# Kernel optimization log

Measured on AMD Instinct MI355X. Metric: run time of the kernel, lower is better.

Reference implementation:

```python
import jax, jax.numpy as jnp
import numpy as np

N = 32768
E = 8           # num_submodules (4x2 grid)
HID = 256       # hidden_dim
POS_DIM = 63    # 3*(1+2*10)
DIR_DIM = 27    # 3*(1+2*4)
APP_DIM = 48
IN_DIM = POS_DIM + APP_DIM        # 111
SKIP_IN = HID + IN_DIM            # 367
COL_IN = HID + DIR_DIM            # 283
COL_HID = HID // 2                # 128
NUM_APP = 1000

SCENE = np.array([-100.0, -100.0, -10.0, 100.0, 100.0, 50.0], np.float32)
_margin = (1.0 - 0.8) / 2.0       # (1 - foreground_ratio)/2
_rng = SCENE[3:] - SCENE[:3]
FG_LO = SCENE[:3] + _rng * _margin
FG_HI = SCENE[3:] - _rng * _margin

def _centroids():
    xs = np.linspace(-100.0, 100.0, 3)   # grid_cols + 1
    ys = np.linspace(-100.0, 100.0, 5)   # grid_rows + 1
    zc = (-10.0 + 50.0) / 2.0
    cs = []
    for i in range(4):
        for j in range(2):
            cs.append([(xs[j] + xs[j + 1]) / 2.0, (ys[i] + ys[i + 1]) / 2.0, zc])
    return np.asarray(cs, np.float32)
CENTROIDS = _centroids()  # [E,3]

def posenc(x, max_log2, num_freqs):
    freqs = (2.0 ** np.linspace(0.0, max_log2, num_freqs)).astype(np.float32)
    parts = [x]
    for f in freqs:
        parts.append(jnp.sin(f * x))
        parts.append(jnp.cos(f * x))
    return jnp.concatenate(parts, axis=-1)

def setup_inputs() -> dict:
    key = jax.random.key(0)
    ks = jax.random.split(key, 24)
    lo, hi = jnp.asarray(SCENE[:3]), jnp.asarray(SCENE[3:])
    points = jax.random.uniform(ks[0], (N, 3), jnp.float32) * (hi - lo) + lo
    vd = jax.random.normal(ks[1], (N, 3), jnp.float32)
    viewdirs = vd / jnp.linalg.norm(vd, axis=-1, keepdims=True)
    appearance_idx = jax.random.randint(ks[2], (N,), 0, NUM_APP, jnp.int32)
    s = 0.02
    p = lambda k, shape: jax.random.normal(k, shape, jnp.float32) * s
    return {
        'points': points, 'viewdirs': viewdirs, 'appearance_idx': appearance_idx,
        'app_embed': p(ks[3], (E, NUM_APP, APP_DIM)),
        'W0': p(ks[4], (E, IN_DIM, HID)),      'b0': p(ks[5], (E, HID)),
        'W_pre': p(ks[6], (E, 3, HID, HID)),   'b_pre': p(ks[7], (E, 3, HID)),
        'Wskip': p(ks[8], (E, SKIP_IN, HID)),  'bskip': p(ks[9], (E, HID)),
        'W_post': p(ks[10], (E, 3, HID, HID)), 'b_post': p(ks[11], (E, 3, HID)),
        'Wd': p(ks[12], (E, HID, 1)),          'bd': p(ks[13], (E, 1)),
        'Wf': p(ks[14], (E, HID, HID)),        'bf': p(ks[15], (E, HID)),
        'Wc1': p(ks[16], (E, COL_IN, COL_HID)),'bc1': p(ks[17], (E, COL_HID)),
        'Wc2': p(ks[18], (E, COL_HID, 3)),     'bc2': p(ks[19], (E, 3)),
    }

def _forward(points, viewdirs, appearance_idx, app_embed, W0, b0, W_pre, b_pre,
             Wskip, bskip, W_post, b_post, Wd, bd, Wf, bf, Wc1, bc1, Wc2, bc2):
    n = points.shape[0]
    cen = jnp.asarray(CENTROIDS)
    fg = jnp.all((points >= jnp.asarray(FG_LO)) & (points <= jnp.asarray(FG_HI)), axis=-1)  # [N]
    # nearest-centroid routing (argmin of L2 == argmin of squared L2)
    expert = jnp.argmin(jnp.sum((points[:, None, :] - cen[None]) ** 2, axis=-1), axis=1)  # [N]
    pe = posenc(points, 10.0, 10)                              # [N,63]
    app = app_embed[:, appearance_idx, :]                      # [E,N,48] per-expert embedding lookup
    x0 = jnp.concatenate([jnp.broadcast_to(pe[None], (E, n, POS_DIM)), app], axis=-1)  # [E,N,111]
    x = jax.nn.relu(jnp.einsum('eni,eih->enh', x0, W0) + b0[:, None])
    for i in range(3):  # linear layers 1..3
        x = jax.nn.relu(jnp.einsum('enh,ehk->enk', x, W_pre[:, i]) + b_pre[:, i][:, None])
    x = jnp.concatenate([x, x0], axis=-1)                      # skip connection at layer 4
    x = jax.nn.relu(jnp.einsum('eni,eih->enh', x, Wskip) + bskip[:, None])
    for i in range(3):  # linear layers 5..7
        x = jax.nn.relu(jnp.einsum('enh,ehk->enk', x, W_post[:, i]) + b_post[:, i][:, None])
    density = jax.nn.relu(jnp.einsum('enh,eho->eno', x, Wd) + bd[:, None])   # [E,N,1]
    feat = jnp.einsum('enh,ehk->enk', x, Wf) + bf[:, None]                   # feature_head (no relu)
    de = posenc(viewdirs, 4.0, 4)                              # [N,27]
    cin = jnp.concatenate([feat, jnp.broadcast_to(de[None], (E, n, DIR_DIM))], axis=-1)  # [E,N,283]
    h = jax.nn.relu(jnp.einsum('eni,eih->enh', cin, Wc1) + bc1[:, None])
    color = jax.nn.sigmoid(jnp.einsum('enh,eho->eno', h, Wc2) + bc2[:, None])  # [E,N,3]
    rows = jnp.arange(n)
    d = jnp.where(fg[:, None], density[expert, rows], 0.0)     # combine: pick routed expert, zero bg
    c = jnp.where(fg[:, None], color[expert, rows], 0.0)
    return d, c

def reference(points, viewdirs, appearance_idx, app_embed, W0, b0, W_pre, b_pre,
              Wskip, bskip, W_post, b_post, Wd, bd, Wf, bf, Wc1, bc1, Wc2, bc2):
    return _forward(points, viewdirs, appearance_idx, app_embed, W0, b0, W_pre, b_pre,
                    Wskip, bskip, W_post, b_post, Wd, bd, Wf, bf, Wc1, bc1, Wc2, bc2)
```

## Files before the change

### kernel.cpp

```cpp
#include <hip/hip_runtime.h>
#include <hip/hip_bf16.h>
#include <math.h>

typedef __bf16 bf16;
typedef __bf16 bf16x4 __attribute__((ext_vector_type(4)));
typedef __bf16 bf16x8 __attribute__((ext_vector_type(8)));
typedef float  f32x4  __attribute__((ext_vector_type(4)));

#define N_PTS 32768

__global__ void k_point(const float* __restrict__ pts, float* __restrict__ out,
                        int* __restrict__ counts, unsigned short* __restrict__ idxlist) {
    __shared__ int lcnt[8], lbase[8];
    int t = threadIdx.x;
    int n = blockIdx.x * 256 + t;
    if (t < 8) lcnt[t] = 0;
    __syncthreads();
    float px = pts[3*n+0], py = pts[3*n+1], pz = pts[3*n+2];
    int e = 0; float best = 3.4e38f;
    #pragma unroll
    for (int i = 0; i < 4; ++i)
        #pragma unroll
        for (int j = 0; j < 2; ++j) {
            float cx = j ? 50.f : -50.f, cy = -75.f + 50.f * i;
            float dx = px - cx, dy = py - cy, dz = pz - 20.f;
            float d = dx*dx + dy*dy + dz*dz;
            if (d < best) { best = d; e = i*2 + j; }
        }
    bool fg = (px >= -80.f && px <= 80.f && py >= -80.f && py <= 80.f &&
               pz >= -4.f  && pz <= 44.f);
    int slot = -1;
    if (fg) {
        slot = atomicAdd(&lcnt[e], 1);
    } else {
        out[n] = 0.f;
        out[N_PTS + 3*n + 0] = 0.f;
        out[N_PTS + 3*n + 1] = 0.f;
        out[N_PTS + 3*n + 2] = 0.f;
    }
    __syncthreads();
    if (t < 8) lbase[t] = atomicAdd(&counts[t], lcnt[t]);
    __syncthreads();
    if (slot >= 0) idxlist[e * N_PTS + lbase[e] + slot] = (unsigned short)n;
}

__global__ void k_tp(const float* __restrict__ s0, const float* __restrict__ s1,
                     const float* __restrict__ s2, const float* __restrict__ s3,
                     const float* __restrict__ s4, const float* __restrict__ s5,
                     bf16* __restrict__ d0, bf16* __restrict__ d1, bf16* __restrict__ d2,
                     bf16* __restrict__ d3, bf16* __restrict__ d4, bf16* __restrict__ d5,
                     const float* __restrict__ pts, float* __restrict__ out,
                     int* __restrict__ counts, unsigned short* __restrict__ idxlist) {
    int t = threadIdx.x;
    if (blockIdx.y == 6) {
        __shared__ int lcnt[8], lbase[8];
        if (blockIdx.x >= N_PTS / 256) return;
        int n = blockIdx.x * 256 + t;
        if (t < 8) lcnt[t] = 0;
        __syncthreads();
        float px = pts[3*n+0], py = pts[3*n+1], pz = pts[3*n+2];
        int e = 0; float best = 3.4e38f;
        #pragma unroll
        for (int i = 0; i < 4; ++i)
            #pragma unroll
            for (int j = 0; j < 2; ++j) {
                float cx = j ? 50.f : -50.f, cy = -75.f + 50.f * i;
                float dx = px - cx, dy = py - cy, dz = pz - 20.f;
                float d = dx*dx + dy*dy + dz*dz;
                if (d < best) { best = d; e = i*2 + j; }
            }
        bool fg = (px >= -80.f && px <= 80.f && py >= -80.f && py <= 80.f &&
                   pz >= -4.f  && pz <= 44.f);
        int slot = -1;
        if (fg) {
            slot = atomicAdd(&lcnt[e], 1);
        } else {
            out[n] = 0.f;
            out[N_PTS + 3*n + 0] = 0.f;
            out[N_PTS + 3*n + 1] = 0.f;
            out[N_PTS + 3*n + 2] = 0.f;
        }
        __syncthreads();
        if (t < 8) lbase[t] = atomicAdd(&counts[t], lcnt[t]);
        __syncthreads();
        if (slot >= 0) idxlist[e * N_PTS + lbase[e] + slot] = (unsigned short)n;
        return;
    }
    __shared__ bf16 tile[64 * 68];
    const float* src; bf16* dst; int K, Nn, Kpad, Eg;
    switch (blockIdx.y) {
        case 0:  src = s0; dst = d0; K = 111; Nn = 256; Kpad = 128; Eg = 8;  break;
        case 1:  src = s1; dst = d1; K = 256; Nn = 256; Kpad = 256; Eg = 24; break;
        case 2:  src = s2; dst = d2; K = 367; Nn = 256; Kpad = 384; Eg = 8;  break;
        case 3:  src = s3; dst = d3; K = 256; Nn = 256; Kpad = 256; Eg = 24; break;
        case 4:  src = s4; dst = d4; K = 256; Nn = 256; Kpad = 256; Eg = 8;  break;
        default: src = s5; dst = d5; K = 283; Nn = 128; Kpad = 288; Eg = 8;  break;
    }
    int ktiles = (Kpad + 63) / 64, ntiles = Nn / 64;
    int b = blockIdx.x;
    if (b >= Eg * ktiles * ntiles) return;
    int eg = b / (ktiles * ntiles), rem = b % (ktiles * ntiles);
    int kt = rem / ntiles, nt = rem % ntiles;
    #pragma unroll
    for (int r = 0; r < 4; ++r) {
        int idx = r * 256 + t;
        int kl = idx >> 4, nl4 = (idx & 15) * 4;
        int kg = kt * 64 + kl, ng = nt * 64 + nl4;
        bf16x4 v = (bf16x4){(bf16)0.f, (bf16)0.f, (bf16)0.f, (bf16)0.f};
        if (kg < K) {
            f32x4 f = *(const f32x4*)(src + ((size_t)(eg * K + kg)) * Nn + ng);
            v[0] = (bf16)f[0]; v[1] = (bf16)f[1]; v[2] = (bf16)f[2]; v[3] = (bf16)f[3];
        }
        *(bf16x4*)(&tile[kl * 68 + nl4]) = v;
    }
    __syncthreads();
    #pragma unroll
    for (int i = 0; i < 2; ++i) {
        int idx = i * 256 + t;
        int ng_l = idx >> 3, kq = idx & 7;
        int kg = kt * 64 + kq * 8, ng = nt * 64 + ng_l;
        if (kg < Kpad) {
            bf16x8 v;
            #pragma unroll
            for (int j = 0; j < 8; ++j) v[j] = tile[(kq * 8 + j) * 68 + ng_l];
            size_t off = ((size_t)(ng >> 5) * (Kpad >> 5) + (size_t)(kg >> 5)) * 1024
                       + (size_t)((ng >> 4) & 1) * 512
                       + (size_t)((kg >> 3) & 3) * 128
                       + (size_t)(ng & 15) * 8;
            *(bf16x8*)(dst + (size_t)eg * Nn * Kpad + off) = v;
        }
    }
}

__device__ __forceinline__ f32x4 mfma16(bf16x8 a, bf16x8 b, f32x4 c) {
    return __builtin_amdgcn_mfma_f32_16x16x32_bf16(a, b, c, 0, 0, 0);
}

__device__ __forceinline__ void zacc(f32x4 acc[2][2]) {
    #pragma unroll
    for (int i = 0; i < 2; ++i)
        #pragma unroll
        for (int j = 0; j < 2; ++j) acc[i][j] = (f32x4){0.f, 0.f, 0.f, 0.f};
}

template<int NS, int KPAD>
__device__ __forceinline__ void gemm_p(f32x4 acc[2][2], const bf16* A, int astr,
                                       const bf16* __restrict__ Wt, int wk0,
                                       int nbase, int l16, int quad, int lane) {
    const bf16* bp = Wt + ((size_t)(nbase >> 5) * (KPAD >> 5) + (size_t)(wk0 >> 5)) * 1024
                   + (size_t)lane * 8;
    __builtin_amdgcn_s_setprio(1);
    #pragma unroll
    for (int s = 0; s < NS; ++s) {
        int kA = s * 32 + quad * 8;
        bf16x8 a0 = *(const bf16x8*)(A + (size_t)(l16)      * astr + kA);
        bf16x8 a1 = *(const bf16x8*)(A + (size_t)(16 + l16) * astr + kA);
        bf16x8 b0 = *(const bf16x8*)(bp + s * 1024);
        bf16x8 b1 = *(const bf16x8*)(bp + s * 1024 + 512);
        acc[0][0] = mfma16(a0, b0, acc[0][0]);
        acc[1][0] = mfma16(a1, b0, acc[1][0]);
        acc[0][1] = mfma16(a0, b1, acc[0][1]);
        acc[1][1] = mfma16(a1, b1, acc[1][1]);
    }
    __builtin_amdgcn_s_setprio(0);
}

template<int NS, bool GUARD>
__device__ __forceinline__ void gemm_g(f32x4 acc[2][2], const bf16* A, int astr,
                                       const float* __restrict__ W, int ldn, int wk0, int Klim,
                                       int nbase, int l16, int quad) {
    #pragma unroll
    for (int s = 0; s < NS; ++s) {
        int kA = s * 32 + quad * 8;
        bf16x8 a0 = *(const bf16x8*)(A + (size_t)(l16)      * astr + kA);
        bf16x8 a1 = *(const bf16x8*)(A + (size_t)(16 + l16) * astr + kA);
        #pragma unroll
        for (int nt = 0; nt < 2; ++nt) {
            int n = nbase + nt * 16 + l16;
            const float* wp = W + (size_t)(wk0 + kA) * ldn + n;
            bf16x8 b;
            #pragma unroll
            for (int j = 0; j < 8; ++j) {
                float wv = 0.f;
                if (!GUARD || (wk0 + kA + j < Klim)) wv = wp[(size_t)j * ldn];
                b[j] = (bf16)wv;
            }
            acc[0][nt] = mfma16(a0, b, acc[0][nt]);
            acc[1][nt] = mfma16(a1, b, acc[1][nt]);
        }
    }
}

__device__ __forceinline__ void epi(f32x4 acc[2][2], const float* bias, bool dorelu,
                                    bf16* dst, int dstr, int nbase, int l16, int quad) {
    #pragma unroll
    for (int nt = 0; nt < 2; ++nt) {
        float bv = bias[nbase + nt * 16 + l16];
        #pragma unroll
        for (int mt = 0; mt < 2; ++mt) {
            #pragma unroll
            for (int r = 0; r < 4; ++r) {
                float v = acc[mt][nt][r] + bv;
                v = fminf(fmaxf(v, -64.f), 64.f);
                if (dorelu) v = fmaxf(v, 0.f);
                dst[(size_t)(mt * 16 + quad * 4 + r) * dstr + nbase + nt * 16 + l16] = (bf16)v;
            }
        }
    }
}

template<bool PACKED>
__global__ __launch_bounds__(512, 2)
void k_main(const int* __restrict__ counts, const unsigned short* __restrict__ idxlist,
            const float* __restrict__ pts, const float* __restrict__ dirs,
            const float* __restrict__ app_embed, const int* __restrict__ aidx,
            const float* __restrict__ W0, const float* __restrict__ b0,
            const float* __restrict__ W_pre, const float* __restrict__ b_pre,
            const float* __restrict__ Wskip, const float* __restrict__ bskip,
            const float* __restrict__ W_post, const float* __restrict__ b_post,
            const float* __restrict__ Wd, const float* __restrict__ bd,
            const float* __restrict__ Wf, const float* __restrict__ bf_,
            const float* __restrict__ Wc1, const float* __restrict__ bc1,
            const float* __restrict__ Wc2, const float* __restrict__ bc2,
            const bf16* __restrict__ wt0, const bf16* __restrict__ wtpre,
            const bf16* __restrict__ wtskip, const bf16* __restrict__ wtpost,
            const bf16* __restrict__ wtf, const bf16* __restrict__ wtc1,
            float* __restrict__ out) {
    __shared__ bf16 xaA[32 * 264];
    __shared__ bf16 xaB[32 * 264];
    __shared__ bf16 x0l[32 * 136];
    __shared__ bf16 del[32 * 48];
    __shared__ int  gidx[32];
    __shared__ int  aid[32];

    const int e    = blockIdx.x & 7;
    const int tile = blockIdx.x >> 3;
    const int cnt  = counts[e];
    if (tile * 32 >= cnt) return;
    const int t = threadIdx.x;
    const int lane = t & 63, wv = t >> 6;
    const int l16 = lane & 15, quad = lane >> 4;
    const int nbase = wv * 32;

    if (t < 32) {
        int i = tile * 32 + t;
        int g = (i < cnt) ? (int)idxlist[e * N_PTS + i] : -1;
        gidx[t] = g;
        aid[t]  = (g >= 0) ? aidx[g] : 0;
    }
    __syncthreads();
    {
        int row = t >> 4, c0 = t & 15, g = gidx[row];
        float p0 = 0.f, p1 = 0.f, p2 = 0.f, q0 = 0.f, q1 = 0.f, q2 = 0.f;
        if (g >= 0) {
            p0 = pts[3*g+0];  p1 = pts[3*g+1];  p2 = pts[3*g+2];
            q0 = dirs[3*g+0]; q1 = dirs[3*g+1]; q2 = dirs[3*g+2];
        }
        int ai = aid[row];
        #pragma unroll
        for (int i = 0; i < 8; ++i) {
            int col = c0 + 16 * i;
            float v = 0.f;
            if (g >= 0 && col < 111) {
                if (col < 3) {
                    v = (col == 0) ? p0 : (col == 1) ? p1 : p2;
                } else if (col < 63) {
                    int q = col - 3, fi = q / 6, d = q % 6, ax = (d < 3) ? d : (d - 3);
                    float p = (ax == 0) ? p0 : (ax == 1) ? p1 : p2;
                    float f = (float)exp2((double)fi * (10.0 / 9.0));
                    v = (d < 3) ? sinf(f * p) : cosf(f * p);
                } else {
                    v = app_embed[((size_t)(e * 1000 + ai)) * 48 + (col - 63)];
                }
            }
            x0l[row * 136 + col] = (bf16)v;
        }
        #pragma unroll
        for (int i = 0; i < 2; ++i) {
            int col = c0 + 16 * i;
            float v = 0.f;
            if (g >= 0 && col < 27) {
                if (col < 3) {
                    v = (col == 0) ? q0 : (col == 1) ? q1 : q2;
                } else {
                    int q = col - 3, fi = q / 6, d = q % 6, ax = (d < 3) ? d : (d - 3);
                    float p = (ax == 0) ? q0 : (ax == 1) ? q1 : q2;
                    float f = (float)exp2((double)fi * (4.0 / 3.0));
                    v = (d < 3) ? sinf(f * p) : cosf(f * p);
                }
            }
            del[row * 48 + col] = (bf16)v;
        }
    }
    __syncthreads();

    f32x4 acc[2][2];
    zacc(acc);
    if (PACKED) gemm_p<4, 128>(acc, x0l, 136, wt0 + (size_t)e * 32768, 0, nbase, l16, quad, lane);
    else        gemm_g<4, true>(acc, x0l, 136, W0 + (size_t)e * 28416, 256, 0, 111, nbase, l16, quad);
    epi(acc, b0 + e * 256, true, xaA, 264, nbase, l16, quad);
    __syncthreads();
    #pragma unroll
    for (int i = 0; i < 3; ++i) {
        const bf16* src = (i & 1) ? xaB : xaA;
        bf16*       dst = (i & 1) ? xaA : xaB;
        zacc(acc);
        if (PACKED) gemm_p<8, 256>(acc, src, 264, wtpre + (size_t)(e * 3 + i) * 65536, 0, nbase, l16, quad, lane);
        else        gemm_g<8, false>(acc, src, 264, W_pre + (size_t)(e * 3 + i) * 65536, 256, 0, 256, nbase, l16, quad);
        epi(acc, b_pre + (e * 3 + i) * 256, true, dst, 264, nbase, l16, quad);
        __syncthreads();
    }
    zacc(acc);
    if (PACKED) {
        gemm_p<8, 384>(acc, xaB, 264, wtskip + (size_t)e * 98304, 0,   nbase, l16, quad, lane);
        gemm_p<4, 384>(acc, x0l, 136, wtskip + (size_t)e * 98304, 256, nbase, l16, quad, lane);
    } else {
        gemm_g<8, false>(acc, xaB, 264, Wskip + (size_t)e * 93952, 256, 0,   367, nbase, l16, quad);
        gemm_g<4, true >(acc, x0l, 136, Wskip + (size_t)e * 93952, 256, 256, 367, nbase, l16, quad);
    }
    epi(acc, bskip + e * 256, true, xaA, 264, nbase, l16, quad);
    __syncthreads();
    #pragma unroll
    for (int i = 0; i < 3; ++i) {
        const bf16* src = (i & 1) ? xaB : xaA;
        bf16*       dst = (i & 1) ? xaA : xaB;
        zacc(acc);
        if (PACKED) gemm_p<8, 256>(acc, src, 264, wtpost + (size_t)(e * 3 + i) * 65536, 0, nbase, l16, quad, lane);
        else        gemm_g<8, false>(acc, src, 264, W_post + (size_t)(e * 3 + i) * 65536, 256, 0, 256, nbase, l16, quad);
        epi(acc, b_post + (e * 3 + i) * 256, true, dst, 264, nbase, l16, quad);
        __syncthreads();
    }
    {
        int m = t >> 4, p = t & 15;
        const bf16*  xr = xaB + (size_t)m * 264;
        const float* wd = Wd + e * 256;
        float s = 0.f;
        #pragma unroll
        for (int kk = 0; kk < 16; ++kk) s += (float)xr[p * 16 + kk] * wd[p * 16 + kk];
        s += __shfl_down(s, 8, 16);
        s += __shfl_down(s, 4, 16);
        s += __shfl_down(s, 2, 16);
        s += __shfl_down(s, 1, 16);
        if (p == 0) {
            int g = gidx[m];
            if (g >= 0) out[g] = fminf(fmaxf(s + bd[e], 0.f), 64.f);
        }
    }
    zacc(acc);
    if (PACKED) gemm_p<8, 256>(acc, xaB, 264, wtf + (size_t)e * 65536, 0, nbase, l16, quad, lane);
    else        gemm_g<8, false>(acc, xaB, 264, Wf + (size_t)e * 65536, 256, 0, 256, nbase, l16, quad);
    epi(acc, bf_ + e * 256, false, xaA, 264, nbase, l16, quad);
    __syncthreads();
    if (wv < 4) {
        zacc(acc);
        if (PACKED) {
            gemm_p<8, 288>(acc, xaA, 264, wtc1 + (size_t)e * 36864, 0,   nbase, l16, quad, lane);
            gemm_p<1, 288>(acc, del, 48,  wtc1 + (size_t)e * 36864, 256, nbase, l16, quad, lane);
        } else {
            gemm_g<8, false>(acc, xaA, 264, Wc1 + (size_t)e * 36224, 128, 0,   283, nbase, l16, quad);
            gemm_g<1, true >(acc, del, 48,  Wc1 + (size_t)e * 36224, 128, 256, 283, nbase, l16, quad);
        }
        epi(acc, bc1 + e * 128, true, xaB, 264, nbase, l16, quad);
    }
    __syncthreads();
    if (t < 96) {
        int m = t & 31, c = t >> 5;
        int g = gidx[m];
        if (g >= 0) {
            const bf16*  xr = xaB + (size_t)m * 264;
            const float* w  = Wc2 + e * 384 + c;
            float s = 0.f;
            for (int k = 0; k < 128; ++k) s += (float)xr[k] * w[k * 3];
            s += bc2[e * 3 + c];
            s = fminf(fmaxf(s, -30.f), 30.f);
            out[N_PTS + 3 * g + c] = 1.f / (1.f + expf(-s));
        }
    }
}

extern "C" void kernel_launch(void* const* d_in, const int* in_sizes, int n_in,
                              void* d_out, int out_size, void* d_ws, size_t ws_size,
                              hipStream_t stream) {
    const float* points    = (const float*)d_in[0];
    const float* viewdirs  = (const float*)d_in[1];
    const int*   aidx      = (const int*)  d_in[2];
    const float* app_embed = (const float*)d_in[3];
    const float* W0        = (const float*)d_in[4];
    const float* b0        = (const float*)d_in[5];
    const float* W_pre     = (const float*)d_in[6];
    const float* b_pre     = (const float*)d_in[7];
    const float* Wskip     = (const float*)d_in[8];
    const float* bskip     = (const float*)d_in[9];
    const float* W_post    = (const float*)d_in[10];
    const float* b_post    = (const float*)d_in[11];
    const float* Wd        = (const float*)d_in[12];
    const float* bd        = (const float*)d_in[13];
    const float* Wf        = (const float*)d_in[14];
    const float* bf_       = (const float*)d_in[15];
    const float* Wc1       = (const float*)d_in[16];
    const float* bc1       = (const float*)d_in[17];
    const float* Wc2       = (const float*)d_in[18];
    const float* bc2       = (const float*)d_in[19];
    float* out = (float*)d_out;
    (void)in_sizes; (void)n_in; (void)out_size;

    char* ws = (char*)d_ws;
    size_t off = 0;
    auto alloc = [&](size_t bytes) -> void* {
        void* p = ws + off;
        off += (bytes + 255) & ~(size_t)255;
        return p;
    };
    int*            counts  = (int*)            alloc(8 * 4);
    unsigned short* idxlist = (unsigned short*) alloc((size_t)8 * N_PTS * 2);
    bf16* wt0    = (bf16*)alloc((size_t)8  * 256 * 128 * 2);
    bf16* wtpre  = (bf16*)alloc((size_t)24 * 256 * 256 * 2);
    bf16* wtskip = (bf16*)alloc((size_t)8  * 256 * 384 * 2);
    bf16* wtpost = (bf16*)alloc((size_t)24 * 256 * 256 * 2);
    bf16* wtf    = (bf16*)alloc((size_t)8  * 256 * 256 * 2);
    bf16* wtc1   = (bf16*)alloc((size_t)8  * 128 * 288 * 2);
    const bool packed = (off <= ws_size);

    hipMemsetAsync(counts, 0, 8 * sizeof(int), stream);
    #define MAIN_ARGS counts, idxlist, points, viewdirs, app_embed, aidx, \
        W0, b0, W_pre, b_pre, Wskip, bskip, W_post, b_post, Wd, bd, Wf, bf_, \
        Wc1, bc1, Wc2, bc2, wt0, wtpre, wtskip, wtpost, wtf, wtc1, out
    if (packed) {
        hipLaunchKernelGGL(k_tp, dim3(384, 7), dim3(256), 0, stream,
                           W0, W_pre, Wskip, W_post, Wf, Wc1,
                           wt0, wtpre, wtskip, wtpost, wtf, wtc1,
                           points, out, counts, idxlist);
        hipLaunchKernelGGL(k_main<true>,  dim3(8 * (N_PTS / 32)), dim3(512), 0, stream, MAIN_ARGS);
    } else {
        hipLaunchKernelGGL(k_point, dim3(N_PTS / 256), dim3(256), 0, stream,
                           points, out, counts, idxlist);
        hipLaunchKernelGGL(k_main<false>, dim3(8 * (N_PTS / 32)), dim3(512), 0, stream, MAIN_ARGS);
    }
    #undef MAIN_ARGS
}
```

Before: 155.4 us.

## Prefetch next layer's packed weights into registers during the epilogue

```diff
diff --git a/kernel.cpp b/kernel.cpp
--- a/kernel.cpp
+++ b/kernel.cpp
@@ -8,6 +8,11 @@
 typedef float  f32x4  __attribute__((ext_vector_type(4)));
 
 #define N_PTS 32768
+
+#define LGKM_BARRIER() do { \
+    asm volatile("s_waitcnt lgkmcnt(0)" ::: "memory"); \
+    __builtin_amdgcn_s_barrier(); \
+} while (0)
 
 __global__ void k_point(const float* __restrict__ pts, float* __restrict__ out,
                         int* __restrict__ counts, unsigned short* __restrict__ idxlist) {
@@ -144,6 +149,34 @@
 }
 
 template<int NS, int KPAD>
+__device__ __forceinline__ void ldpf(bf16x8 pf[16], const bf16* __restrict__ Wt,
+                                     int nbase, int lane) {
+    const bf16* bp = Wt + ((size_t)(nbase >> 5) * (KPAD >> 5)) * 1024 + (size_t)lane * 8;
+    #pragma unroll
+    for (int s = 0; s < NS; ++s) {
+        pf[s * 2]     = *(const bf16x8*)(bp + s * 1024);
+        pf[s * 2 + 1] = *(const bf16x8*)(bp + s * 1024 + 512);
+    }
+}
+
+template<int NS>
+__device__ __forceinline__ void gemm_pf(f32x4 acc[2][2], const bf16* A, int astr,
+                                        const bf16x8 (&pf)[16], int l16, int quad) {
+    __builtin_amdgcn_s_setprio(1);
+    #pragma unroll
+    for (int s = 0; s < NS; ++s) {
+        int kA = s * 32 + quad * 8;
+        bf16x8 a0 = *(const bf16x8*)(A + (size_t)(l16)      * astr + kA);
+        bf16x8 a1 = *(const bf16x8*)(A + (size_t)(16 + l16) * astr + kA);
+        acc[0][0] = mfma16(a0, pf[s*2],   acc[0][0]);
+        acc[1][0] = mfma16(a1, pf[s*2],   acc[1][0]);
+        acc[0][1] = mfma16(a0, pf[s*2+1], acc[0][1]);
+        acc[1][1] = mfma16(a1, pf[s*2+1], acc[1][1]);
+    }
+    __builtin_amdgcn_s_setprio(0);
+}
+
+template<int NS, int KPAD>
 __device__ __forceinline__ void gemm_p(f32x4 acc[2][2], const bf16* A, int astr,
                                        const bf16* __restrict__ Wt, int wk0,
                                        int nbase, int l16, int quad, int lane) {
@@ -210,7 +243,7 @@
 }
 
 template<bool PACKED>
-__global__ __launch_bounds__(512, 2)
+__global__ __launch_bounds__(512, 4)
 void k_main(const int* __restrict__ counts, const unsigned short* __restrict__ idxlist,
             const float* __restrict__ pts, const float* __restrict__ dirs,
             const float* __restrict__ app_embed, const int* __restrict__ aidx,
@@ -242,13 +275,17 @@
     const int l16 = lane & 15, quad = lane >> 4;
     const int nbase = wv * 32;
 
+    f32x4  acc[2][2];
+    bf16x8 pf[16];
+    if (PACKED) ldpf<4, 128>(pf, wt0 + (size_t)e * 32768, nbase, lane);
+
     if (t < 32) {
         int i = tile * 32 + t;
         int g = (i < cnt) ? (int)idxlist[e * N_PTS + i] : -1;
         gidx[t] = g;
         aid[t]  = (g >= 0) ? aidx[g] : 0;
     }
-    __syncthreads();
+    LGKM_BARRIER();
     {
         int row = t >> 4, c0 = t & 15, g = gidx[row];
         float p0 = 0.f, p1 = 0.f, p2 = 0.f, q0 = 0.f, q1 = 0.f, q2 = 0.f;
@@ -292,43 +329,57 @@
             del[row * 48 + col] = (bf16)v;
         }
     }
-    __syncthreads();
-
-    f32x4 acc[2][2];
+    LGKM_BARRIER();
+
     zacc(acc);
-    if (PACKED) gemm_p<4, 128>(acc, x0l, 136, wt0 + (size_t)e * 32768, 0, nbase, l16, quad, lane);
-    else        gemm_g<4, true>(acc, x0l, 136, W0 + (size_t)e * 28416, 256, 0, 111, nbase, l16, quad);
+    if (PACKED) {
+        gemm_pf<4>(acc, x0l, 136, pf, l16, quad);
+        ldpf<8, 256>(pf, wtpre + (size_t)(e * 3) * 65536, nbase, lane);
+    } else {
+        gemm_g<4, true>(acc, x0l, 136, W0 + (size_t)e * 28416, 256, 0, 111, nbase, l16, quad);
+    }
     epi(acc, b0 + e * 256, true, xaA, 264, nbase, l16, quad);
-    __syncthreads();
+    LGKM_BARRIER();
     #pragma unroll
     for (int i = 0; i < 3; ++i) {
         const bf16* src = (i & 1) ? xaB : xaA;
         bf16*       dst = (i & 1) ? xaA : xaB;
         zacc(acc);
-        if (PACKED) gemm_p<8, 256>(acc, src, 264, wtpre + (size_t)(e * 3 + i) * 65536, 0, nbase, l16, quad, lane);
-        else        gemm_g<8, false>(acc, src, 264, W_pre + (size_t)(e * 3 + i) * 65536, 256, 0, 256, nbase, l16, quad);
+        if (PACKED) {
+            gemm_pf<8>(acc, src, 264, pf, l16, quad);
+            if (i < 2) ldpf<8, 256>(pf, wtpre + (size_t)(e * 3 + i + 1) * 65536, nbase, lane);
+            else       ldpf<8, 384>(pf, wtskip + (size_t)e * 98304, nbase, lane);
+        } else {
+            gemm_g<8, false>(acc, src, 264, W_pre + (size_t)(e * 3 + i) * 65536, 256, 0, 256, nbase, l16, quad);
+        }
         epi(acc, b_pre + (e * 3 + i) * 256, true, dst, 264, nbase, l16, quad);
-        __syncthreads();
+        LGKM_BARRIER();
     }
     zacc(acc);
     if (PACKED) {
-        gemm_p<8, 384>(acc, xaB, 264, wtskip + (size_t)e * 98304, 0,   nbase, l16, quad, lane);
+        gemm_pf<8>(acc, xaB, 264, pf, l16, quad);
         gemm_p<4, 384>(acc, x0l, 136, wtskip + (size_t)e * 98304, 256, nbase, l16, quad, lane);
+        ldpf<8, 256>(pf, wtpost + (size_t)(e * 3) * 65536, nbase, lane);
     } else {
         gemm_g<8, false>(acc, xaB, 264, Wskip + (size_t)e * 93952, 256, 0,   367, nbase, l16, quad);
         gemm_g<4, true >(acc, x0l, 136, Wskip + (size_t)e * 93952, 256, 256, 367, nbase, l16, quad);
     }
     epi(acc, bskip + e * 256, true, xaA, 264, nbase, l16, quad);
-    __syncthreads();
+    LGKM_BARRIER();
     #pragma unroll
     for (int i = 0; i < 3; ++i) {
         const bf16* src = (i & 1) ? xaB : xaA;
         bf16*       dst = (i & 1) ? xaA : xaB;
         zacc(acc);
-        if (PACKED) gemm_p<8, 256>(acc, src, 264, wtpost + (size_t)(e * 3 + i) * 65536, 0, nbase, l16, quad, lane);
-        else        gemm_g<8, false>(acc, src, 264, W_post + (size_t)(e * 3 + i) * 65536, 256, 0, 256, nbase, l16, quad);
+        if (PACKED) {
+            gemm_pf<8>(acc, src, 264, pf, l16, quad);
+            if (i < 2) ldpf<8, 256>(pf, wtpost + (size_t)(e * 3 + i + 1) * 65536, nbase, lane);
+            else       ldpf<8, 256>(pf, wtf + (size_t)e * 65536, nbase, lane);
+        } else {
+            gemm_g<8, false>(acc, src, 264, W_post + (size_t)(e * 3 + i) * 65536, 256, 0, 256, nbase, l16, quad);
+        }
         epi(acc, b_post + (e * 3 + i) * 256, true, dst, 264, nbase, l16, quad);
-        __syncthreads();
+        LGKM_BARRIER();
     }
     {
         int m = t >> 4, p = t & 15;
@@ -347,22 +398,26 @@
         }
     }
     zacc(acc);
-    if (PACKED) gemm_p<8, 256>(acc, xaB, 264, wtf + (size_t)e * 65536, 0, nbase, l16, quad, lane);
-    else        gemm_g<8, false>(acc, xaB, 264, Wf + (size_t)e * 65536, 256, 0, 256, nbase, l16, quad);
+    if (PACKED) {
+        gemm_pf<8>(acc, xaB, 264, pf, l16, quad);
+        if (wv < 4) ldpf<8, 288>(pf, wtc1 + (size_t)e * 36864, nbase, lane);
+    } else {
+        gemm_g<8, false>(acc, xaB, 264, Wf + (size_t)e * 65536, 256, 0, 256, nbase, l16, quad);
+    }
     epi(acc, bf_ + e * 256, false, xaA, 264, nbase, l16, quad);
-    __syncthreads();
+    LGKM_BARRIER();
     if (wv < 4) {
         zacc(acc);
         if (PACKED) {
-            gemm_p<8, 288>(acc, xaA, 264, wtc1 + (size_t)e * 36864, 0,   nbase, l16, quad, lane);
-            gemm_p<1, 288>(acc, del, 48,  wtc1 + (size_t)e * 36864, 256, nbase, l16, quad, lane);
+            gemm_pf<8>(acc, xaA, 264, pf, l16, quad);
+            gemm_p<1, 288>(acc, del, 48, wtc1 + (size_t)e * 36864, 256, nbase, l16, quad, lane);
         } else {
             gemm_g<8, false>(acc, xaA, 264, Wc1 + (size_t)e * 36224, 128, 0,   283, nbase, l16, quad);
             gemm_g<1, true >(acc, del, 48,  Wc1 + (size_t)e * 36224, 128, 256, 283, nbase, l16, quad);
         }
         epi(acc, bc1 + e * 128, true, xaB, 264, nbase, l16, quad);
     }
-    __syncthreads();
+    LGKM_BARRIER();
     if (t < 96) {
         int m = t & 31, c = t >> 5;
         int g = gidx[m];
```

Result: slower. 164.7 us (+6.0%).
